# Kernel tuning notes

Measured on AMD Instinct MI355X. Metric: run time of the kernel, lower is better.

The kernel has to match this reference:

```python
import jax, jax.numpy as jnp
import numpy as np

GROUPS = 4
KLD_SCALE = 10.0
COMMITMENT_COST = 0.25


def setup_inputs() -> dict:
    key = jax.random.key(0)
    k1, k2 = jax.random.split(key)
    z = jax.random.normal(k1, (8, 4096, 512), dtype=jnp.float32)
    embed_w = jax.random.normal(k2, (512, 128), dtype=jnp.float32)
    return {"z": z, "embed_w": embed_w}


def reference(z, embed_w):
    B, N, D = z.shape
    d = D // GROUPS  # sub-vector dim per group
    flat = z.reshape(B * N * GROUPS, d)  # [M, d]
    # squared euclidean distance to each codebook entry: [M, K]
    dist = (
        jnp.sum(flat * flat, axis=1, keepdims=True)
        - 2.0 * flat @ embed_w.T
        + jnp.sum(embed_w * embed_w, axis=1)[None, :]
    )
    ind = jnp.argmin(dist, axis=1)  # argmax(-dist)
    z_q = embed_w[ind]  # [M, d] codebook gather
    sg = jax.lax.stop_gradient
    diff = KLD_SCALE * (
        COMMITMENT_COST * jnp.mean((sg(z_q) - flat) ** 2)
        + jnp.mean((z_q - sg(flat)) ** 2)
    )
    # straight-through estimator
    z_q_st = (flat + sg(z_q - flat)).reshape(B, N, D)
    ind_out = ind.reshape(N, B, GROUPS)  # matches torch .view on contiguous buffer
    return (z_q_st, diff, ind_out)
```

## Files before the change

kernel.cpp:

```cpp
#include <hip/hip_runtime.h>
#include <float.h>


typedef __attribute__((ext_vector_type(8))) short short8;
typedef __attribute__((ext_vector_type(4))) float f32x4;

constexpr int Dn = 128;
constexpr int K  = 512;
constexpr long long Mrows = 131072;
constexpr int RPB  = 128;
constexpr int NBLK = (int)(Mrows / RPB);
constexpr int CHUNK = 32;
constexpr int NCH   = K / CHUNK;
constexpr float TAU_A = 0.004f;

constexpr size_t ZQ_SIZE  = (size_t)Mrows * Dn;
constexpr size_t DIFF_OFF = ZQ_SIZE;
constexpr size_t IND_OFF  = ZQ_SIZE + 1;

__device__ inline unsigned short f2bf(float f) {
    unsigned u = __builtin_bit_cast(unsigned, f);
    u += 0x7FFFu + ((u >> 16) & 1u);
    return (unsigned short)(u >> 16);
}
__device__ inline float bf2f(unsigned short s) {
    unsigned u = ((unsigned)s) << 16;
    return __builtin_bit_cast(float, u);
}

__device__ inline void gload_lds16(const void* g, void* l) {
    __builtin_amdgcn_global_load_lds(
        (const __attribute__((address_space(1))) unsigned int*)g,
        (__attribute__((address_space(3))) unsigned int*)l,
        16, 0, 0);
}

__global__ void wnorm_kernel(const float* __restrict__ W, float* __restrict__ wn2) {
    int k = blockIdx.x * blockDim.x + threadIdx.x;
    if (k < K) {
        double s = 0.0;
        const float* w = W + (size_t)k * Dn;
        #pragma unroll 4
        for (int i = 0; i < Dn; ++i) { double v = (double)w[i]; s += v * v; }
        wn2[k] = (float)(-0.5 * s);
    }
}

__global__ void prep_kernel(const float* __restrict__ W, unsigned short* __restrict__ Wp) {
    int t = blockIdx.x * 256 + threadIdx.x;
    int code   = t >> 4;
    int gs     = t & 15;
    int ch     = code >> 5;
    int code_l = code & 31;
    int g      = gs ^ (code_l & 7);
    const float* src = W + (size_t)code * Dn + g * 8;
    ushort4 h[2], l[2];
    #pragma unroll
    for (int half = 0; half < 2; ++half) {
        float4 v = *(const float4*)(src + half * 4);
        float vv[4] = {v.x, v.y, v.z, v.w};
        unsigned short* hp = (unsigned short*)&h[half];
        unsigned short* lp = (unsigned short*)&l[half];
        #pragma unroll
        for (int e = 0; e < 4; ++e) {
            unsigned short hs = f2bf(vv[e]);
            hp[e] = hs;
            lp[e] = f2bf(vv[e] - bf2f(hs));
        }
    }
    size_t base = (size_t)ch * 8192 + (size_t)(code_l * 16 + gs) * 8;
    *(ushort4*)(Wp + base)            = h[0];
    *(ushort4*)(Wp + base + 4)        = h[1];
    *(ushort4*)(Wp + base + 4096)     = l[0];
    *(ushort4*)(Wp + base + 4096 + 4) = l[1];
}

__global__ __launch_bounds__(256, 4) void vq_main(
        const float* __restrict__ Z, const float* __restrict__ W,
        const unsigned short* __restrict__ Wp, const float* __restrict__ wn2,
        float* __restrict__ out, double* __restrict__ diffsum) {
    __shared__ __align__(16) char Wbuf[2][16384];
    __shared__ float wn2_s[K];
    __shared__ int   sIdx[RPB];
    __shared__ int   sFlag[RPB];
    __shared__ float xn_s[RPB];
    __shared__ float wpart[4];

    const int tid  = threadIdx.x;
    const int w    = tid >> 6;
    const int lane = tid & 63;
    const int lm   = lane & 15;
    const int lg   = lane >> 4;
    const size_t row0 = (size_t)blockIdx.x * RPB;

    auto stage = [&](int bi, int ch) {
        const char* gsrc = (const char*)Wp + (size_t)ch * 16384;
        char* lb = &Wbuf[bi][0];
        #pragma unroll
        for (int it = 0; it < 4; ++it) {
            const int gb = (w * 4 + it) * 64;
            gload_lds16(gsrc + (size_t)(gb + lane) * 16, lb + (size_t)gb * 16);
        }
    };
    stage(0, 0);

    short8 ahi[2][4], alo[2][4];
    #pragma unroll
    for (int r = 0; r < 2; ++r) {
        const size_t grow = row0 + (size_t)w * 32 + r * 16 + lm;
        float s2 = 0.f;
        #pragma unroll
        for (int ks = 0; ks < 4; ++ks) {
            const float* xp = Z + grow * Dn + ks * 32 + lg * 8;
            float4 x0 = *(const float4*)xp;
            float4 x1 = *(const float4*)(xp + 4);
            float xv[8] = {x0.x, x0.y, x0.z, x0.w, x1.x, x1.y, x1.z, x1.w};
            #pragma unroll
            for (int j = 0; j < 8; ++j) {
                unsigned short hs = f2bf(xv[j]);
                ahi[r][ks][j] = (short)hs;
                alo[r][ks][j] = (short)f2bf(xv[j] - bf2f(hs));
                s2 += xv[j] * xv[j];
            }
        }
        s2 += __shfl_xor(s2, 16);
        s2 += __shfl_xor(s2, 32);
        if (lg == 0) xn_s[w * 32 + r * 16 + lm] = s2;
    }
    #pragma unroll
    for (int i = 0; i < K / 256; ++i) wn2_s[tid + i * 256] = wn2[tid + i * 256];

    float m1[2][4], m2[2][4];
    int   i1[2][4];
    #pragma unroll
    for (int r = 0; r < 2; ++r)
        #pragma unroll
        for (int j = 0; j < 4; ++j) { m1[r][j] = -FLT_MAX; m2[r][j] = -FLT_MAX; i1[r][j] = 0; }

    asm volatile("s_waitcnt vmcnt(0)" ::: "memory");
    __syncthreads();

    for (int ch = 0; ch < NCH; ++ch) {
        const int cur = ch & 1;
        if (ch + 1 < NCH) stage(cur ^ 1, ch + 1);
        const char* buf = &Wbuf[cur][0];

        #pragma unroll
        for (int t = 0; t < 2; ++t) {
            const int code_l = t * 16 + lm;
            const int c = ch * CHUNK + code_l;
            const float cinit = wn2_s[c];
            short8 bhi[4], blo[4];
            #pragma unroll
            for (int ks = 0; ks < 4; ++ks) {
                const int off = code_l * 256 + ((((ks << 2) + lg) ^ (code_l & 7)) << 4);
                bhi[ks] = *(const short8*)(buf + off);
                blo[ks] = *(const short8*)(buf + 8192 + off);
            }
            f32x4 acc[2];
            #pragma unroll
            for (int r = 0; r < 2; ++r) acc[r] = (f32x4){cinit, cinit, cinit, cinit};
            #pragma unroll
            for (int ks = 0; ks < 4; ++ks) {
                #pragma unroll
                for (int r = 0; r < 2; ++r) {
                    acc[r] = __builtin_amdgcn_mfma_f32_16x16x32_bf16(ahi[r][ks], bhi[ks], acc[r], 0, 0, 0);
                    acc[r] = __builtin_amdgcn_mfma_f32_16x16x32_bf16(alo[r][ks], bhi[ks], acc[r], 0, 0, 0);
                    acc[r] = __builtin_amdgcn_mfma_f32_16x16x32_bf16(ahi[r][ks], blo[ks], acc[r], 0, 0, 0);
                }
            }
            #pragma unroll
            for (int r = 0; r < 2; ++r) {
                #pragma unroll
                for (int j = 0; j < 4; ++j) {
                    const float a = acc[r][j];
                    m2[r][j] = __builtin_amdgcn_fmed3f(a, m1[r][j], m2[r][j]);
                    const bool gt = a > m1[r][j];
                    m1[r][j] = fmaxf(m1[r][j], a);
                    i1[r][j] = gt ? c : i1[r][j];
                }
            }
        }
        asm volatile("s_waitcnt vmcnt(0)" ::: "memory");
        __syncthreads();
    }

    #pragma unroll
    for (int sft = 1; sft < 16; sft <<= 1) {
        #pragma unroll
        for (int r = 0; r < 2; ++r) {
            #pragma unroll
            for (int j = 0; j < 4; ++j) {
                float o1 = __shfl_xor(m1[r][j], sft);
                float o2 = __shfl_xor(m2[r][j], sft);
                int   oi = __shfl_xor(i1[r][j], sft);
                if (o1 > m1[r][j] || (o1 == m1[r][j] && oi < i1[r][j])) {
                    m2[r][j] = fmaxf(m1[r][j], o2);
                    m1[r][j] = o1;
                    i1[r][j] = oi;
                } else {
                    m2[r][j] = fmaxf(m2[r][j], o1);
                }
            }
        }
    }

    float psum = 0.f;
    if (lm == 0) {
        #pragma unroll
        for (int r = 0; r < 2; ++r) {
            #pragma unroll
            for (int j = 0; j < 4; ++j) {
                const int row = w * 32 + r * 16 + lg * 4 + j;
                sIdx[row]  = i1[r][j];
                sFlag[row] = (m1[r][j] - m2[r][j] < TAU_A) ? 1 : 0;
                psum += xn_s[row] - 2.f * m1[r][j];
            }
        }
    }
    __syncthreads();

    {
        const int rbase = w * 32;
        unsigned long long fl = __ballot(lane < 32 && sFlag[rbase + (lane & 31)]);
        while (fl) {
            const int rr = rbase + (__ffsll(fl) - 1);
            fl &= fl - 1;
            const float* xp = Z + (row0 + rr) * Dn;
            double best = 1e300; int bi = 0;
            for (int jj = 0; jj < 8; ++jj) {
                const int k = lane + 64 * jj;
                const float* wp = W + (size_t)k * Dn;
                double s = 0.0;
                for (int i = 0; i < Dn; ++i) {
                    double dx = (double)xp[i] - (double)wp[i];
                    s += dx * dx;
                }
                if (s < best) { best = s; bi = k; }
            }
            #pragma unroll
            for (int sft = 1; sft < 64; sft <<= 1) {
                double ob = __shfl_xor(best, sft);
                int    ok = __shfl_xor(bi, sft);
                if (ob < best || (ob == best && ok < bi)) { best = ob; bi = ok; }
            }
            if (lane == 0) sIdx[rr] = bi;
        }
    }
    __syncthreads();

    #pragma unroll
    for (int it = 0; it < 16; ++it) {
        int f4i = tid + it * 256;
        int row = f4i >> 5, cq = f4i & 31;
        int ind = sIdx[row];
        float4 wv = ((const float4*)(W + (size_t)ind * Dn))[cq];
        ((float4*)(out + (row0 + row) * Dn))[cq] = wv;
    }
    if (tid < RPB) out[IND_OFF + row0 + tid] = (float)sIdx[tid];

    #pragma unroll
    for (int sft = 1; sft < 64; sft <<= 1) psum += __shfl_xor(psum, sft);
    if (lane == 0) wpart[w] = psum;
    __syncthreads();
    if (tid == 0) {
        double t = (double)wpart[0] + (double)wpart[1] + (double)wpart[2] + (double)wpart[3];
        atomicAdd(diffsum, t);
    }
}

__global__ void diff_kernel(const double* __restrict__ diffsum, float* __restrict__ out) {
    if (threadIdx.x == 0 && blockIdx.x == 0) {
        out[DIFF_OFF] = (float)(12.5 * diffsum[0] / (double)ZQ_SIZE);
    }
}

extern "C" void kernel_launch(void* const* d_in, const int* in_sizes, int n_in,
                              void* d_out, int out_size, void* d_ws, size_t ws_size,
                              hipStream_t stream) {
    (void)in_sizes; (void)n_in; (void)out_size; (void)ws_size;
    const float* Z = (const float*)d_in[0];
    const float* W = (const float*)d_in[1];
    float* out = (float*)d_out;
    double* diffsum = (double*)d_ws;
    float* wn2 = (float*)((char*)d_ws + 16);
    unsigned short* Wp = (unsigned short*)((char*)d_ws + 4096);

    hipMemsetAsync(d_ws, 0, 16, stream);
    wnorm_kernel<<<2, 256, 0, stream>>>(W, wn2);
    prep_kernel<<<32, 256, 0, stream>>>(W, Wp);
    vq_main<<<NBLK, 256, 0, stream>>>(Z, W, Wp, wn2, out, diffsum);
    diff_kernel<<<1, 64, 0, stream>>>(diffsum, out);
}
```

Baseline: 135.9 us.

## Switch distance GEMM to fp16 two-term split and 64 rows per wave

Replaces the three-MFMA bf16 hi/lo split with fp16, where activations use a single fp16 term and the codebook keeps a hi/lo pair. Each distance tile then needs two MFMAs instead of three. Blocks shrink to two waves of 64 rows each, so every codebook LDS fragment is reused across four row tiles. The near-tie threshold rises so that more rows fall back to the exact fp64 recheck, offsetting the lower activation precision at the cost of extra fallback work; fewer waves per block also changes occupancy.

```diff
diff --git a/kernel.cpp b/kernel.cpp
--- a/kernel.cpp
+++ b/kernel.cpp
@@ -2,31 +2,23 @@
 #include <float.h>
 
 
-typedef __attribute__((ext_vector_type(8))) short short8;
+typedef _Float16 half8 __attribute__((ext_vector_type(8)));
 typedef __attribute__((ext_vector_type(4))) float f32x4;
 
 constexpr int Dn = 128;
 constexpr int K  = 512;
 constexpr long long Mrows = 131072;
-constexpr int RPB  = 128;
+constexpr int RPW  = 64;
+constexpr int WAVES = 2;
+constexpr int RPB  = RPW * WAVES;
 constexpr int NBLK = (int)(Mrows / RPB);
 constexpr int CHUNK = 32;
 constexpr int NCH   = K / CHUNK;
-constexpr float TAU_A = 0.004f;
+constexpr float TAU_A = 0.02f;
 
 constexpr size_t ZQ_SIZE  = (size_t)Mrows * Dn;
 constexpr size_t DIFF_OFF = ZQ_SIZE;
 constexpr size_t IND_OFF  = ZQ_SIZE + 1;
-
-__device__ inline unsigned short f2bf(float f) {
-    unsigned u = __builtin_bit_cast(unsigned, f);
-    u += 0x7FFFu + ((u >> 16) & 1u);
-    return (unsigned short)(u >> 16);
-}
-__device__ inline float bf2f(unsigned short s) {
-    unsigned u = ((unsigned)s) << 16;
-    return __builtin_bit_cast(float, u);
-}
 
 __device__ inline void gload_lds16(const void* g, void* l) {
     __builtin_amdgcn_global_load_lds(
@@ -63,9 +55,10 @@
         unsigned short* lp = (unsigned short*)&l[half];
         #pragma unroll
         for (int e = 0; e < 4; ++e) {
-            unsigned short hs = f2bf(vv[e]);
-            hp[e] = hs;
-            lp[e] = f2bf(vv[e] - bf2f(hs));
+            _Float16 hh = (_Float16)vv[e];
+            _Float16 ll = (_Float16)(vv[e] - (float)hh);
+            hp[e] = __builtin_bit_cast(unsigned short, hh);
+            lp[e] = __builtin_bit_cast(unsigned short, ll);
         }
     }
     size_t base = (size_t)ch * 8192 + (size_t)(code_l * 16 + gs) * 8;
@@ -75,7 +68,7 @@
     *(ushort4*)(Wp + base + 4096 + 4) = l[1];
 }
 
-__global__ __launch_bounds__(256, 4) void vq_main(
+__global__ __launch_bounds__(128) void vq_main(
         const float* __restrict__ Z, const float* __restrict__ W,
         const unsigned short* __restrict__ Wp, const float* __restrict__ wn2,
         float* __restrict__ out, double* __restrict__ diffsum) {
@@ -84,7 +77,7 @@
     __shared__ int   sIdx[RPB];
     __shared__ int   sFlag[RPB];
     __shared__ float xn_s[RPB];
-    __shared__ float wpart[4];
+    __shared__ float wpart[WAVES];
 
     const int tid  = threadIdx.x;
     const int w    = tid >> 6;
@@ -97,17 +90,17 @@
         const char* gsrc = (const char*)Wp + (size_t)ch * 16384;
         char* lb = &Wbuf[bi][0];
         #pragma unroll
-        for (int it = 0; it < 4; ++it) {
-            const int gb = (w * 4 + it) * 64;
+        for (int it = 0; it < 8; ++it) {
+            const int gb = (w * 8 + it) * 64;
             gload_lds16(gsrc + (size_t)(gb + lane) * 16, lb + (size_t)gb * 16);
         }
     };
     stage(0, 0);
 
-    short8 ahi[2][4], alo[2][4];
-    #pragma unroll
-    for (int r = 0; r < 2; ++r) {
-        const size_t grow = row0 + (size_t)w * 32 + r * 16 + lm;
+    half8 ah[4][4];
+    #pragma unroll
+    for (int r = 0; r < 4; ++r) {
+        const size_t grow = row0 + (size_t)w * RPW + r * 16 + lm;
         float s2 = 0.f;
         #pragma unroll
         for (int ks = 0; ks < 4; ++ks) {
@@ -117,23 +110,21 @@
             float xv[8] = {x0.x, x0.y, x0.z, x0.w, x1.x, x1.y, x1.z, x1.w};
             #pragma unroll
             for (int j = 0; j < 8; ++j) {
-                unsigned short hs = f2bf(xv[j]);
-                ahi[r][ks][j] = (short)hs;
-                alo[r][ks][j] = (short)f2bf(xv[j] - bf2f(hs));
+                ah[r][ks][j] = (_Float16)xv[j];
                 s2 += xv[j] * xv[j];
             }
         }
         s2 += __shfl_xor(s2, 16);
         s2 += __shfl_xor(s2, 32);
-        if (lg == 0) xn_s[w * 32 + r * 16 + lm] = s2;
-    }
-    #pragma unroll
-    for (int i = 0; i < K / 256; ++i) wn2_s[tid + i * 256] = wn2[tid + i * 256];
-
-    float m1[2][4], m2[2][4];
-    int   i1[2][4];
-    #pragma unroll
-    for (int r = 0; r < 2; ++r)
+        if (lg == 0) xn_s[w * RPW + r * 16 + lm] = s2;
+    }
+    #pragma unroll
+    for (int i = 0; i < K / 128; ++i) wn2_s[tid + i * 128] = wn2[tid + i * 128];
+
+    float m1[4][4], m2[4][4];
+    int   i1[4][4];
+    #pragma unroll
+    for (int r = 0; r < 4; ++r)
         #pragma unroll
         for (int j = 0; j < 4; ++j) { m1[r][j] = -FLT_MAX; m2[r][j] = -FLT_MAX; i1[r][j] = 0; }
 
@@ -150,27 +141,26 @@
             const int code_l = t * 16 + lm;
             const int c = ch * CHUNK + code_l;
             const float cinit = wn2_s[c];
-            short8 bhi[4], blo[4];
+            half8 bh[4], bl[4];
             #pragma unroll
             for (int ks = 0; ks < 4; ++ks) {
                 const int off = code_l * 256 + ((((ks << 2) + lg) ^ (code_l & 7)) << 4);
-                bhi[ks] = *(const short8*)(buf + off);
-                blo[ks] = *(const short8*)(buf + 8192 + off);
-            }
-            f32x4 acc[2];
-            #pragma unroll
-            for (int r = 0; r < 2; ++r) acc[r] = (f32x4){cinit, cinit, cinit, cinit};
+                bh[ks] = *(const half8*)(buf + off);
+                bl[ks] = *(const half8*)(buf + 8192 + off);
+            }
+            f32x4 acc[4];
+            #pragma unroll
+            for (int r = 0; r < 4; ++r) acc[r] = (f32x4){cinit, cinit, cinit, cinit};
             #pragma unroll
             for (int ks = 0; ks < 4; ++ks) {
                 #pragma unroll
-                for (int r = 0; r < 2; ++r) {
-                    acc[r] = __builtin_amdgcn_mfma_f32_16x16x32_bf16(ahi[r][ks], bhi[ks], acc[r], 0, 0, 0);
-                    acc[r] = __builtin_amdgcn_mfma_f32_16x16x32_bf16(alo[r][ks], bhi[ks], acc[r], 0, 0, 0);
-                    acc[r] = __builtin_amdgcn_mfma_f32_16x16x32_bf16(ahi[r][ks], blo[ks], acc[r], 0, 0, 0);
-                }
-            }
-            #pragma unroll
-            for (int r = 0; r < 2; ++r) {
+                for (int r = 0; r < 4; ++r) {
+                    acc[r] = __builtin_amdgcn_mfma_f32_16x16x32_f16(ah[r][ks], bh[ks], acc[r], 0, 0, 0);
+                    acc[r] = __builtin_amdgcn_mfma_f32_16x16x32_f16(ah[r][ks], bl[ks], acc[r], 0, 0, 0);
+                }
+            }
+            #pragma unroll
+            for (int r = 0; r < 4; ++r) {
                 #pragma unroll
                 for (int j = 0; j < 4; ++j) {
                     const float a = acc[r][j];
@@ -188,7 +178,7 @@
     #pragma unroll
     for (int sft = 1; sft < 16; sft <<= 1) {
         #pragma unroll
-        for (int r = 0; r < 2; ++r) {
+        for (int r = 0; r < 4; ++r) {
             #pragma unroll
             for (int j = 0; j < 4; ++j) {
                 float o1 = __shfl_xor(m1[r][j], sft);
@@ -208,10 +198,10 @@
     float psum = 0.f;
     if (lm == 0) {
         #pragma unroll
-        for (int r = 0; r < 2; ++r) {
+        for (int r = 0; r < 4; ++r) {
             #pragma unroll
             for (int j = 0; j < 4; ++j) {
-                const int row = w * 32 + r * 16 + lg * 4 + j;
+                const int row = w * RPW + r * 16 + lg * 4 + j;
                 sIdx[row]  = i1[r][j];
                 sFlag[row] = (m1[r][j] - m2[r][j] < TAU_A) ? 1 : 0;
                 psum += xn_s[row] - 2.f * m1[r][j];
@@ -221,8 +211,8 @@
     __syncthreads();
 
     {
-        const int rbase = w * 32;
-        unsigned long long fl = __ballot(lane < 32 && sFlag[rbase + (lane & 31)]);
+        const int rbase = w * RPW;
+        unsigned long long fl = __ballot(sFlag[rbase + lane] != 0);
         while (fl) {
             const int rr = rbase + (__ffsll(fl) - 1);
             fl &= fl - 1;
@@ -250,21 +240,21 @@
     __syncthreads();
 
     #pragma unroll
-    for (int it = 0; it < 16; ++it) {
-        int f4i = tid + it * 256;
+    for (int it = 0; it < 32; ++it) {
+        int f4i = tid + it * 128;
         int row = f4i >> 5, cq = f4i & 31;
         int ind = sIdx[row];
         float4 wv = ((const float4*)(W + (size_t)ind * Dn))[cq];
         ((float4*)(out + (row0 + row) * Dn))[cq] = wv;
     }
-    if (tid < RPB) out[IND_OFF + row0 + tid] = (float)sIdx[tid];
+    out[IND_OFF + row0 + tid] = (float)sIdx[tid];
 
     #pragma unroll
     for (int sft = 1; sft < 64; sft <<= 1) psum += __shfl_xor(psum, sft);
     if (lane == 0) wpart[w] = psum;
     __syncthreads();
     if (tid == 0) {
-        double t = (double)wpart[0] + (double)wpart[1] + (double)wpart[2] + (double)wpart[3];
+        double t = (double)wpart[0] + (double)wpart[1];
         atomicAdd(diffsum, t);
     }
 }
@@ -289,6 +279,6 @@
     hipMemsetAsync(d_ws, 0, 16, stream);
     wnorm_kernel<<<2, 256, 0, stream>>>(W, wn2);
     prep_kernel<<<32, 256, 0, stream>>>(W, Wp);
-    vq_main<<<NBLK, 256, 0, stream>>>(Z, W, Wp, wn2, out, diffsum);
+    vq_main<<<NBLK, 128, 0, stream>>>(Z, W, Wp, wn2, out, diffsum);
     diff_kernel<<<1, 64, 0, stream>>>(diffsum, out);
 }
```

Result: slower. 173.7 us (+27.8%).
